# Kernel optimization log

Hardware: AMD Instinct MI355X
Metric: run time of the kernel (lower is better)

Reference implementation:

```python
import jax, jax.numpy as jnp
import numpy as np

Q, N, D = 4096, 50000, 64

def setup_inputs() -> dict:
    key = jax.random.key(0)
    k1, k2, k3, k4 = jax.random.split(key, 4)
    features = jax.random.normal(k1, (Q, D), dtype=jnp.float32)
    # bw_transform is a (lower-triangular cholesky) bandwidth transform; a small
    # random matrix is fine for a numerical reference. Scale down so exp(-d2/2)
    # does not underflow everywhere.
    bw_transform = jax.random.normal(k2, (D, D), dtype=jnp.float32) * 0.05
    dataset = jax.random.normal(k3, (N, D), dtype=jnp.float32)
    norm = jax.random.uniform(k4, (1,), dtype=jnp.float32)
    return {"features": features, "bw_transform": bw_transform, "dataset": dataset, "norm": norm}

def reference(features, bw_transform, dataset, norm):
    # features: [Q, D], bw_transform: [D, D], dataset: [N, D] (already transformed), norm: [1]
    f = features @ bw_transform  # [Q, D]
    # pairwise squared distances via expansion: ||f||^2 + ||x||^2 - 2 f.x
    f2 = jnp.sum(f * f, axis=1)            # [Q]
    x2 = jnp.sum(dataset * dataset, axis=1)  # [N]
    d2 = f2[:, None] + x2[None, :] - 2.0 * (f @ dataset.T)  # [Q, N]
    kern = jnp.exp(-0.5 * d2) * norm[0]    # [Q, N]
    estimate = jnp.mean(kern, axis=1)       # [Q]
    return estimate
```

## Files before the change

kernel.cpp:

```cpp
#include <hip/hip_runtime.h>


#define QCNT 4096
#define NCNT 50000
#define DDIM 64

#define SPLITS 64
#define NPB 832
#define NROWS (SPLITS * NPB)
#define NHALVES 52
#define QTILES (QCNT / 256)
#define SPLIT_HALVES (NPB * DDIM)

#define FSPLITS 32
#define FNPB 1563
#define FNITERS 25
#define BN 64

typedef _Float16 half8_t __attribute__((ext_vector_type(8)));
typedef float float4_t __attribute__((ext_vector_type(4)));

#define K2F 1.44269504088896340f
#define KC2 -0.72134752044448169f

#define PREP_F_BLOCKS (QCNT / 4)
#define PREP_X_BLOCKS (NROWS * 8 / 256)

__global__ void prep_fused(const float* __restrict__ features,
                           const float* __restrict__ bw,
                           const float* __restrict__ dataset,
                           _Float16* __restrict__ fh,
                           float* __restrict__ cf2,
                           _Float16* __restrict__ xhp,
                           float* __restrict__ ecxg) {
    if (blockIdx.x < PREP_F_BLOCKS) {
        const int lane = threadIdx.x & 63;
        const int q = blockIdx.x * 4 + (threadIdx.x >> 6);
        const float* frow = features + q * DDIM;
        float acc = 0.f;
#pragma unroll
        for (int k = 0; k < DDIM; ++k)
            acc = fmaf(frow[k], bw[k * DDIM + lane], acc);
        fh[(size_t)q * DDIM + lane] = (_Float16)(K2F * acc);
        float s = acc * acc;
#pragma unroll
        for (int m = 1; m < 64; m <<= 1) s += __shfl_xor(s, m, 64);
        if (lane == 0) cf2[q] = KC2 * s;
    } else {
        const int t = (blockIdx.x - PREP_F_BLOCKS) * 256 + threadIdx.x;
        const int row = t >> 3;
        const int c = t & 7;
        if (row >= NROWS) return;
        float4_t v0 = {0.f, 0.f, 0.f, 0.f}, v1 = {0.f, 0.f, 0.f, 0.f};
        if (row < NCNT) {
            const float4_t* src = (const float4_t*)(dataset + (size_t)row * DDIM + c * 8);
            v0 = src[0]; v1 = src[1];
        }
        float s = v0[0]*v0[0] + v0[1]*v0[1] + v0[2]*v0[2] + v0[3]*v0[3]
                + v1[0]*v1[0] + v1[1]*v1[1] + v1[2]*v1[2] + v1[3]*v1[3];
        s += __shfl_xor(s, 1, 64);
        s += __shfl_xor(s, 2, 64);
        s += __shfl_xor(s, 4, 64);
        if (c == 0) ecxg[row] = (row < NCNT) ? __builtin_amdgcn_exp2f(KC2 * s) : 0.f;
        half8_t h;
        h[0] = (_Float16)v0[0]; h[1] = (_Float16)v0[1];
        h[2] = (_Float16)v0[2]; h[3] = (_Float16)v0[3];
        h[4] = (_Float16)v1[0]; h[5] = (_Float16)v1[1];
        h[6] = (_Float16)v1[2]; h[7] = (_Float16)v1[3];
        const int split = row / NPB;
        const int nr = row - split * NPB;
        const int hh = nr >> 4;
        const int l15 = nr & 15;
        const int f = c >> 2;
        const int lh = c & 3;
        const int lane = lh * 16 + l15;
        const size_t base = (((size_t)split * NHALVES + hh) * 2 + f) * 512;
        *(half8_t*)(xhp + base + lane * 8) = h;
    }
}

__global__ __attribute__((amdgpu_flat_work_group_size(256, 256),
                          amdgpu_waves_per_eu(4, 4)))
void kde_main_fast(const _Float16* __restrict__ fh,
                   const float* __restrict__ ecxg,
                   const _Float16* __restrict__ xhp,
                   float* __restrict__ partial) {
    __shared__ float lecx[NPB];

    const int tid = threadIdx.x;
    const int lane = tid & 63;
    const int w = tid >> 6;
    const int l15 = lane & 15;
    const int lh = lane >> 4;

    const int bid = blockIdx.x;
    const int xcd = bid & 7;
    const int j = bid >> 3;
    const int split = xcd * 8 + (j & 7);
    const int qtile = j >> 3;

    const int qbase = qtile * 256 + w * 64;

    half8_t a[4][2];
#pragma unroll
    for (int qt = 0; qt < 4; ++qt)
#pragma unroll
        for (int kt = 0; kt < 2; ++kt)
            a[qt][kt] = *(const half8_t*)(fh + (size_t)(qbase + qt * 16 + l15) * DDIM
                                             + kt * 32 + lh * 8);

    {
        const float* es = ecxg + (size_t)split * NPB;
        for (int i = tid; i < NPB; i += 256) lecx[i] = es[i];
    }
    __syncthreads();

    {
        const int skew = w + ((bid >> 3) & 3);
#pragma unroll 1
        for (int i = 0; i < skew; ++i) __builtin_amdgcn_s_sleep(2);
    }

    const _Float16* bs = xhp + (size_t)split * SPLIT_HALVES + (size_t)lane * 8;

    float sum[4][4];
#pragma unroll
    for (int qt = 0; qt < 4; ++qt)
#pragma unroll
        for (int r = 0; r < 4; ++r) sum[qt][r] = 0.f;

    const float4_t zc = {0.f, 0.f, 0.f, 0.f};

#define LOADH(L, h_)                                                          \
    {                                                                         \
        const _Float16* p_ = bs + (size_t)(h_) * 1024;                        \
        L[0] = *(const half8_t*)(p_);                                         \
        L[1] = *(const half8_t*)(p_ + 512);                                   \
    }

#define MFMAH(T, L)                                                           \
    {                                                                         \
        __builtin_amdgcn_s_setprio(1);                                        \
        T[0] = __builtin_amdgcn_mfma_f32_16x16x32_f16(a[0][0], L[0], zc, 0, 0, 0); \
        T[1] = __builtin_amdgcn_mfma_f32_16x16x32_f16(a[1][0], L[0], zc, 0, 0, 0); \
        T[2] = __builtin_amdgcn_mfma_f32_16x16x32_f16(a[2][0], L[0], zc, 0, 0, 0); \
        T[3] = __builtin_amdgcn_mfma_f32_16x16x32_f16(a[3][0], L[0], zc, 0, 0, 0); \
        T[0] = __builtin_amdgcn_mfma_f32_16x16x32_f16(a[0][1], L[1], T[0], 0, 0, 0); \
        T[1] = __builtin_amdgcn_mfma_f32_16x16x32_f16(a[1][1], L[1], T[1], 0, 0, 0); \
        T[2] = __builtin_amdgcn_mfma_f32_16x16x32_f16(a[2][1], L[1], T[2], 0, 0, 0); \
        T[3] = __builtin_amdgcn_mfma_f32_16x16x32_f16(a[3][1], L[1], T[3], 0, 0, 0); \
        __builtin_amdgcn_s_setprio(0);                                        \
    }

#define EXPH(T, h_)                                                           \
    {                                                                         \
        const float e_ = lecx[(h_) * 16 + l15];                               \
        _Pragma("unroll")                                                     \
        for (int r = 0; r < 4; ++r) {                                         \
            sum[0][r] = fmaf(__builtin_amdgcn_exp2f(T[0][r]), e_, sum[0][r]); \
            sum[1][r] = fmaf(__builtin_amdgcn_exp2f(T[1][r]), e_, sum[1][r]); \
            sum[2][r] = fmaf(__builtin_amdgcn_exp2f(T[2][r]), e_, sum[2][r]); \
            sum[3][r] = fmaf(__builtin_amdgcn_exp2f(T[3][r]), e_, sum[3][r]); \
        }                                                                     \
    }

    half8_t lA[2], lB[2];
    float4_t tA[4], tB[4];

    LOADH(lA, 0);
    LOADH(lB, 1);
    MFMAH(tA, lA);
    LOADH(lA, 2);

#pragma unroll 1
    for (int h = 0; h < NHALVES - 4; h += 2) {
        MFMAH(tB, lB);
        EXPH(tA, h);
        LOADH(lB, h + 3);
        MFMAH(tA, lA);
        EXPH(tB, h + 1);
        LOADH(lA, h + 4);
    }
    MFMAH(tB, lB);
    EXPH(tA, 48);
    LOADH(lB, 51);
    MFMAH(tA, lA);
    EXPH(tB, 49);
    MFMAH(tB, lB);
    EXPH(tA, 50);
    EXPH(tB, 51);

#pragma unroll
    for (int qt = 0; qt < 4; ++qt)
#pragma unroll
        for (int r = 0; r < 4; ++r) {
            float s = sum[qt][r];
            s += __shfl_xor(s, 1, 64);
            s += __shfl_xor(s, 2, 64);
            s += __shfl_xor(s, 4, 64);
            s += __shfl_xor(s, 8, 64);
            sum[qt][r] = s;
        }
    if (l15 == 0) {
        float* dst = partial + (size_t)split * QCNT + qbase;
#pragma unroll
        for (int qt = 0; qt < 4; ++qt)
#pragma unroll
            for (int r = 0; r < 4; ++r)
                dst[qt * 16 + lh * 4 + r] = sum[qt][r];
    }
#undef LOADH
#undef MFMAH
#undef EXPH
}

__global__ void prep_f_kernel(const float* __restrict__ features,
                              const float* __restrict__ bw,
                              _Float16* __restrict__ fh,
                              float* __restrict__ cf2) {
    const int lane = threadIdx.x & 63;
    const int q = blockIdx.x * (blockDim.x >> 6) + (threadIdx.x >> 6);
    if (q >= QCNT) return;
    const float* frow = features + q * DDIM;
    float acc = 0.f;
#pragma unroll
    for (int k = 0; k < DDIM; ++k)
        acc = fmaf(frow[k], bw[k * DDIM + lane], acc);
    fh[(size_t)q * DDIM + lane] = (_Float16)(K2F * acc);
    float s = acc * acc;
#pragma unroll
    for (int m = 1; m < 64; m <<= 1) s += __shfl_xor(s, m, 64);
    if (lane == 0) cf2[q] = KC2 * s;
}

__global__ void prep_x2_kernel(const float* __restrict__ dataset,
                               float* __restrict__ cx2) {
    const int n = blockIdx.x * blockDim.x + threadIdx.x;
    if (n >= NCNT) return;
    const float4* row = (const float4*)(dataset + (size_t)n * DDIM);
    float s = 0.f;
#pragma unroll
    for (int jq = 0; jq < DDIM / 4; ++jq) {
        float4 v = row[jq];
        s += v.x * v.x + v.y * v.y + v.z * v.z + v.w * v.w;
    }
    cx2[n] = KC2 * s;
}

__global__ __launch_bounds__(256, 2)
void kde_main_fb(const _Float16* __restrict__ fh,
                 const float* __restrict__ cx2,
                 const float* __restrict__ dataset,
                 float* __restrict__ partial) {
    __shared__ __align__(16) _Float16 xt[BN * DDIM];
    const int tid = threadIdx.x;
    const int lane = tid & 63;
    const int w = tid >> 6;
    const int l15 = lane & 15;
    const int lh = lane >> 4;
    const int qbase = blockIdx.x * 256 + w * 64;
    const int nstart = blockIdx.y * FNPB;
    const int nlimit = min(nstart + FNPB, NCNT);

    half8_t a[4][2];
#pragma unroll
    for (int qt = 0; qt < 4; ++qt)
#pragma unroll
        for (int kt = 0; kt < 2; ++kt)
            a[qt][kt] = *(const half8_t*)(fh + (size_t)(qbase + qt * 16 + l15) * DDIM
                                             + kt * 32 + lh * 8);
    float sum[4][4];
#pragma unroll
    for (int qt = 0; qt < 4; ++qt)
#pragma unroll
        for (int r = 0; r < 4; ++r) sum[qt][r] = 0.f;

    const int sn = tid >> 2;
    const int sk = tid & 3;
    const int c0 = (sk * 2) ^ (sn & 7);
    const int c1 = (sk * 2 + 1) ^ (sn & 7);

    for (int it = 0; it < FNITERS; ++it) {
        const int nb = nstart + it * BN;
        __syncthreads();
        {
            const int ng = nb + sn;
            float4_t v0 = {0.f,0.f,0.f,0.f}, v1 = {0.f,0.f,0.f,0.f};
            float4_t v2 = {0.f,0.f,0.f,0.f}, v3 = {0.f,0.f,0.f,0.f};
            if (ng < nlimit) {
                const float4_t* src = (const float4_t*)(dataset + (size_t)ng * DDIM + sk * 16);
                v0 = src[0]; v1 = src[1]; v2 = src[2]; v3 = src[3];
            }
            half8_t h0, h1;
            h0[0]=(_Float16)v0[0]; h0[1]=(_Float16)v0[1]; h0[2]=(_Float16)v0[2]; h0[3]=(_Float16)v0[3];
            h0[4]=(_Float16)v1[0]; h0[5]=(_Float16)v1[1]; h0[6]=(_Float16)v1[2]; h0[7]=(_Float16)v1[3];
            h1[0]=(_Float16)v2[0]; h1[1]=(_Float16)v2[1]; h1[2]=(_Float16)v2[2]; h1[3]=(_Float16)v2[3];
            h1[4]=(_Float16)v3[0]; h1[5]=(_Float16)v3[1]; h1[6]=(_Float16)v3[2]; h1[7]=(_Float16)v3[3];
            *(half8_t*)(xt + sn * DDIM + c0 * 8) = h0;
            *(half8_t*)(xt + sn * DDIM + c1 * 8) = h1;
        }
        __syncthreads();
#pragma unroll
        for (int nt = 0; nt < 4; ++nt) {
            const int ng = nb + nt * 16 + l15;
            const float c2 = (ng < nlimit) ? cx2[ng] : -1.0e30f;
            const int brow = nt * 16 + l15;
            const half8_t b0 = *(const half8_t*)(xt + brow * DDIM + ((lh ^ (brow & 7)) * 8));
            const half8_t b1 = *(const half8_t*)(xt + brow * DDIM + (((4 + lh) ^ (brow & 7)) * 8));
#pragma unroll
            for (int qt = 0; qt < 4; ++qt) {
                float4_t c = {c2, c2, c2, c2};
                float4_t acc = __builtin_amdgcn_mfma_f32_16x16x32_f16(a[qt][0], b0, c, 0, 0, 0);
                acc = __builtin_amdgcn_mfma_f32_16x16x32_f16(a[qt][1], b1, acc, 0, 0, 0);
#pragma unroll
                for (int r = 0; r < 4; ++r)
                    sum[qt][r] += __builtin_amdgcn_exp2f(acc[r]);
            }
        }
    }
#pragma unroll
    for (int qt = 0; qt < 4; ++qt)
#pragma unroll
        for (int r = 0; r < 4; ++r) {
            float s = sum[qt][r];
            s += __shfl_xor(s, 1, 64);
            s += __shfl_xor(s, 2, 64);
            s += __shfl_xor(s, 4, 64);
            s += __shfl_xor(s, 8, 64);
            sum[qt][r] = s;
        }
    if (l15 == 0) {
        float* dst = partial + (size_t)blockIdx.y * QCNT + qbase;
#pragma unroll
        for (int qt = 0; qt < 4; ++qt)
#pragma unroll
            for (int r = 0; r < 4; ++r)
                dst[qt * 16 + lh * 4 + r] = sum[qt][r];
    }
}

__global__ void reduce_kernel(const float* __restrict__ partial,
                              const float* __restrict__ cf2,
                              const float* __restrict__ norm,
                              float* __restrict__ out, int splits) {
    const int t = blockIdx.x * blockDim.x + threadIdx.x;
    const int q = t >> 2;
    const int sub = t & 3;
    if (q >= QCNT) return;
    const int per = splits >> 2;
    float s = 0.f;
    for (int sp = sub * per; sp < (sub + 1) * per; ++sp)
        s += partial[(size_t)sp * QCNT + q];
    s += __shfl_xor(s, 1, 64);
    s += __shfl_xor(s, 2, 64);
    if (sub == 0)
        out[q] = s * __builtin_amdgcn_exp2f(cf2[q]) * norm[0] * (1.0f / (float)NCNT);
}

extern "C" void kernel_launch(void* const* d_in, const int* in_sizes, int n_in,
                              void* d_out, int out_size, void* d_ws, size_t ws_size,
                              hipStream_t stream) {
    const float* features = (const float*)d_in[0];
    const float* bw       = (const float*)d_in[1];
    const float* dataset  = (const float*)d_in[2];
    const float* norm     = (const float*)d_in[3];
    float* out = (float*)d_out;
    float* ws = (float*)d_ws;

    const size_t NEED = (size_t)(1703936 + 131072 + 4096 + 53248 + 262144) * 4;

    if (ws_size >= NEED) {
        _Float16* xhp = (_Float16*)ws;
        _Float16* fh  = (_Float16*)(ws + 1703936);
        float* cf2     = ws + 1703936 + 131072;
        float* ecxg    = cf2 + 4096;
        float* partial = ecxg + 53248;

        prep_fused<<<PREP_F_BLOCKS + PREP_X_BLOCKS, 256, 0, stream>>>(
            features, bw, dataset, fh, cf2, xhp, ecxg);
        kde_main_fast<<<QTILES * SPLITS, 256, 0, stream>>>(fh, ecxg, xhp, partial);
        reduce_kernel<<<(QCNT * 4) / 256, 256, 0, stream>>>(partial, cf2, norm, out, SPLITS);
    } else {
        _Float16* fh = (_Float16*)ws;
        float* cf2     = ws + 131072;
        float* cx2     = ws + 131072 + 4096;
        float* partial = ws + 131072 + 4096 + 50176;

        prep_f_kernel<<<QCNT / 4, 256, 0, stream>>>(features, bw, fh, cf2);
        prep_x2_kernel<<<(NCNT + 255) / 256, 256, 0, stream>>>(dataset, cx2);
        dim3 grid(QCNT / 256, FSPLITS);
        kde_main_fb<<<grid, 256, 0, stream>>>(fh, cx2, dataset, partial);
        reduce_kernel<<<(QCNT * 4) / 256, 256, 0, stream>>>(partial, cf2, norm, out, FSPLITS);
    }
}
```

Before: 54.97 us.

## Split kde main kernel into producer MFMA waves and consumer exp waves via LDS

```diff
diff --git a/kernel.cpp b/kernel.cpp
--- a/kernel.cpp
+++ b/kernel.cpp
@@ -79,17 +79,19 @@
     }
 }
 
-__global__ __attribute__((amdgpu_flat_work_group_size(256, 256),
-                          amdgpu_waves_per_eu(4, 4)))
+__global__ __launch_bounds__(512, 2)
 void kde_main_fast(const _Float16* __restrict__ fh,
                    const float* __restrict__ ecxg,
                    const _Float16* __restrict__ xhp,
                    float* __restrict__ partial) {
+    __shared__ __align__(16) float accbuf[2 * 4 * 4 * 64 * 4];
     __shared__ float lecx[NPB];
 
     const int tid = threadIdx.x;
     const int lane = tid & 63;
-    const int w = tid >> 6;
+    const int wv = tid >> 6;
+    const bool producer = wv < 4;
+    const int g = wv & 3;
     const int l15 = lane & 15;
     const int lh = lane >> 4;
 
@@ -99,26 +101,21 @@
     const int split = xcd * 8 + (j & 7);
     const int qtile = j >> 3;
 
-    const int qbase = qtile * 256 + w * 64;
+    const int qbase = qtile * 256 + g * 64;
 
     half8_t a[4][2];
-#pragma unroll
-    for (int qt = 0; qt < 4; ++qt)
-#pragma unroll
-        for (int kt = 0; kt < 2; ++kt)
-            a[qt][kt] = *(const half8_t*)(fh + (size_t)(qbase + qt * 16 + l15) * DDIM
-                                             + kt * 32 + lh * 8);
+    if (producer) {
+#pragma unroll
+        for (int qt = 0; qt < 4; ++qt)
+#pragma unroll
+            for (int kt = 0; kt < 2; ++kt)
+                a[qt][kt] = *(const half8_t*)(fh + (size_t)(qbase + qt * 16 + l15) * DDIM
+                                                 + kt * 32 + lh * 8);
+    }
 
     {
         const float* es = ecxg + (size_t)split * NPB;
-        for (int i = tid; i < NPB; i += 256) lecx[i] = es[i];
-    }
-    __syncthreads();
-
-    {
-        const int skew = w + ((bid >> 3) & 3);
-#pragma unroll 1
-        for (int i = 0; i < skew; ++i) __builtin_amdgcn_s_sleep(2);
+        for (int i = tid; i < NPB; i += 512) lecx[i] = es[i];
     }
 
     const _Float16* bs = xhp + (size_t)split * SPLIT_HALVES + (size_t)lane * 8;
@@ -138,80 +135,93 @@
         L[1] = *(const half8_t*)(p_ + 512);                                   \
     }
 
-#define MFMAH(T, L)                                                           \
+#define PRODUCE(h_, L)                                                        \
     {                                                                         \
+        float4_t t0, t1, t2, t3;                                              \
         __builtin_amdgcn_s_setprio(1);                                        \
-        T[0] = __builtin_amdgcn_mfma_f32_16x16x32_f16(a[0][0], L[0], zc, 0, 0, 0); \
-        T[1] = __builtin_amdgcn_mfma_f32_16x16x32_f16(a[1][0], L[0], zc, 0, 0, 0); \
-        T[2] = __builtin_amdgcn_mfma_f32_16x16x32_f16(a[2][0], L[0], zc, 0, 0, 0); \
-        T[3] = __builtin_amdgcn_mfma_f32_16x16x32_f16(a[3][0], L[0], zc, 0, 0, 0); \
-        T[0] = __builtin_amdgcn_mfma_f32_16x16x32_f16(a[0][1], L[1], T[0], 0, 0, 0); \
-        T[1] = __builtin_amdgcn_mfma_f32_16x16x32_f16(a[1][1], L[1], T[1], 0, 0, 0); \
-        T[2] = __builtin_amdgcn_mfma_f32_16x16x32_f16(a[2][1], L[1], T[2], 0, 0, 0); \
-        T[3] = __builtin_amdgcn_mfma_f32_16x16x32_f16(a[3][1], L[1], T[3], 0, 0, 0); \
+        t0 = __builtin_amdgcn_mfma_f32_16x16x32_f16(a[0][0], L[0], zc, 0, 0, 0); \
+        t1 = __builtin_amdgcn_mfma_f32_16x16x32_f16(a[1][0], L[0], zc, 0, 0, 0); \
+        t2 = __builtin_amdgcn_mfma_f32_16x16x32_f16(a[2][0], L[0], zc, 0, 0, 0); \
+        t3 = __builtin_amdgcn_mfma_f32_16x16x32_f16(a[3][0], L[0], zc, 0, 0, 0); \
+        t0 = __builtin_amdgcn_mfma_f32_16x16x32_f16(a[0][1], L[1], t0, 0, 0, 0); \
+        t1 = __builtin_amdgcn_mfma_f32_16x16x32_f16(a[1][1], L[1], t1, 0, 0, 0); \
+        t2 = __builtin_amdgcn_mfma_f32_16x16x32_f16(a[2][1], L[1], t2, 0, 0, 0); \
+        t3 = __builtin_amdgcn_mfma_f32_16x16x32_f16(a[3][1], L[1], t3, 0, 0, 0); \
         __builtin_amdgcn_s_setprio(0);                                        \
-    }
-
-#define EXPH(T, h_)                                                           \
+        float* ab_ = accbuf + ((((h_) & 1) * 4 + g) * 4 * 64 + lane) * 4;     \
+        *(float4_t*)(ab_ +   0) = t0;                                         \
+        *(float4_t*)(ab_ + 256) = t1;           \
+        *(float4_t*)(ab_ + 512) = t2;                                         \
+        *(float4_t*)(ab_ + 768) = t3;                                         \
+    }
+
+#define CONSUME(h_)                                                           \
     {                                                                         \
         const float e_ = lecx[(h_) * 16 + l15];                               \
+        const float* ab_ = accbuf + ((((h_) & 1) * 4 + g) * 4 * 64 + lane) * 4; \
+        float4_t q0 = *(const float4_t*)(ab_ +   0);                          \
+        float4_t q1 = *(const float4_t*)(ab_ + 256);                          \
+        float4_t q2 = *(const float4_t*)(ab_ + 512);                          \
+        float4_t q3 = *(const float4_t*)(ab_ + 768);                          \
         _Pragma("unroll")                                                     \
         for (int r = 0; r < 4; ++r) {                                         \
-            sum[0][r] = fmaf(__builtin_amdgcn_exp2f(T[0][r]), e_, sum[0][r]); \
-            sum[1][r] = fmaf(__builtin_amdgcn_exp2f(T[1][r]), e_, sum[1][r]); \
-            sum[2][r] = fmaf(__builtin_amdgcn_exp2f(T[2][r]), e_, sum[2][r]); \
-            sum[3][r] = fmaf(__builtin_amdgcn_exp2f(T[3][r]), e_, sum[3][r]); \
+            sum[0][r] = fmaf(__builtin_amdgcn_exp2f(q0[r]), e_, sum[0][r]);   \
+            sum[1][r] = fmaf(__builtin_amdgcn_exp2f(q1[r]), e_, sum[1][r]);   \
+            sum[2][r] = fmaf(__builtin_amdgcn_exp2f(q2[r]), e_, sum[2][r]);   \
+            sum[3][r] = fmaf(__builtin_amdgcn_exp2f(q3[r]), e_, sum[3][r]);   \
         }                                                                     \
     }
 
     half8_t lA[2], lB[2];
-    float4_t tA[4], tB[4];
-
-    LOADH(lA, 0);
-    LOADH(lB, 1);
-    MFMAH(tA, lA);
-    LOADH(lA, 2);
+
+    if (producer) {
+        LOADH(lA, 0);
+        PRODUCE(0, lA);
+        LOADH(lB, 1);
+    }
+    __syncthreads();
 
 #pragma unroll 1
-    for (int h = 0; h < NHALVES - 4; h += 2) {
-        MFMAH(tB, lB);
-        EXPH(tA, h);
-        LOADH(lB, h + 3);
-        MFMAH(tA, lA);
-        EXPH(tB, h + 1);
-        LOADH(lA, h + 4);
-    }
-    MFMAH(tB, lB);
-    EXPH(tA, 48);
-    LOADH(lB, 51);
-    MFMAH(tA, lA);
-    EXPH(tB, 49);
-    MFMAH(tB, lB);
-    EXPH(tA, 50);
-    EXPH(tB, 51);
-
-#pragma unroll
-    for (int qt = 0; qt < 4; ++qt)
-#pragma unroll
-        for (int r = 0; r < 4; ++r) {
-            float s = sum[qt][r];
-            s += __shfl_xor(s, 1, 64);
-            s += __shfl_xor(s, 2, 64);
-            s += __shfl_xor(s, 4, 64);
-            s += __shfl_xor(s, 8, 64);
-            sum[qt][r] = s;
-        }
-    if (l15 == 0) {
-        float* dst = partial + (size_t)split * QCNT + qbase;
+    for (int h = 0; h < NHALVES - 1; ++h) {
+        if (producer) {
+            if ((h & 1) == 0) {
+                PRODUCE(h + 1, lB);
+                if (h + 2 < NHALVES) LOADH(lA, h + 2);
+            } else {
+                PRODUCE(h + 1, lA);
+                if (h + 2 < NHALVES) LOADH(lB, h + 2);
+            }
+        } else {
+            CONSUME(h);
+        }
+        __syncthreads();
+    }
+    if (!producer) CONSUME(NHALVES - 1);
+
+    if (!producer) {
 #pragma unroll
         for (int qt = 0; qt < 4; ++qt)
 #pragma unroll
-            for (int r = 0; r < 4; ++r)
-                dst[qt * 16 + lh * 4 + r] = sum[qt][r];
+            for (int r = 0; r < 4; ++r) {
+                float s = sum[qt][r];
+                s += __shfl_xor(s, 1, 64);
+                s += __shfl_xor(s, 2, 64);
+                s += __shfl_xor(s, 4, 64);
+                s += __shfl_xor(s, 8, 64);
+                sum[qt][r] = s;
+            }
+        if (l15 == 0) {
+            float* dst = partial + (size_t)split * QCNT + qbase;
+#pragma unroll
+            for (int qt = 0; qt < 4; ++qt)
+#pragma unroll
+                for (int r = 0; r < 4; ++r)
+                    dst[qt * 16 + lh * 4 + r] = sum[qt][r];
+        }
     }
 #undef LOADH
-#undef MFMAH
-#undef EXPH
+#undef PRODUCE
+#undef CONSUME
 }
 
 __global__ void prep_f_kernel(const float* __restrict__ features,
@@ -378,7 +388,7 @@
 
         prep_fused<<<PREP_F_BLOCKS + PREP_X_BLOCKS, 256, 0, stream>>>(
             features, bw, dataset, fh, cf2, xhp, ecxg);
-        kde_main_fast<<<QTILES * SPLITS, 256, 0, stream>>>(fh, ecxg, xhp, partial);
+        kde_main_fast<<<QTILES * SPLITS, 512, 0, stream>>>(fh, ecxg, xhp, partial);
         reduce_kernel<<<(QCNT * 4) / 256, 256, 0, stream>>>(partial, cf2, norm, out, SPLITS);
     } else {
         _Float16* fh = (_Float16*)ws;
```

After: 71.70 us. +30.4%, slower.
